# Kernel tuning notes

Hardware: AMD Instinct MI355X
Metric: run time of the kernel (lower is better)

The kernel has to match this reference:

```python
import jax, jax.numpy as jnp
import numpy as np
import math

EMBED_DIM = 128
NUM_HEADS = 16
HEAD_DIM = EMBED_DIM // NUM_HEADS  # = 8 = n_wires of the quantum circuit


def setup_inputs() -> dict:
    key = jax.random.key(0)
    k1, k2, k3 = jax.random.split(key, 3)
    B, S = 4, 2048
    x = jax.random.normal(k1, (B, S, EMBED_DIM), dtype=jnp.float32)
    # shared trainable RX angles of the single q_layer (applied to every head)
    theta = jax.random.normal(k2, (HEAD_DIM,), dtype=jnp.float32)
    w_out = jax.random.normal(k3, (EMBED_DIM, EMBED_DIM), dtype=jnp.float32) / math.sqrt(EMBED_DIM)
    mask = jnp.ones((B, S), dtype=jnp.int32)
    return {"x": x, "theta": theta, "w_out": w_out, "mask": mask}


def quantum_linear(x_head, theta):
    # Circuit: RX(x_i) encode + RX(theta_i) on wire i, CNOT chain (i, i+1),
    # then <Z_j>. For product state |psi_i> = RX(phi_i)|0>, <Z_i> = cos(phi_i),
    # and the CNOT chain gives final <Z_j> = prod_{i<=j} cos(phi_i).
    phi = x_head + theta  # [..., D] broadcast over leading dims
    return jnp.cumprod(jnp.cos(phi), axis=-1)


def reference(x, theta, w_out, mask):
    B, S, E = x.shape
    H, D = NUM_HEADS, HEAD_DIM
    xs = x.reshape(B, S, H, D)
    q = quantum_linear(xs, theta).transpose(0, 2, 1, 3)  # [B, H, S, D]; k = v = q
    scores = jnp.einsum("bhsd,bhtd->bhst", q, q) / math.sqrt(D)
    scores = jnp.where(mask[:, None, None, :] == 0, -1e9, scores)
    probs = jax.nn.softmax(scores, axis=-1)  # dropout is identity in eval
    attn = jnp.einsum("bhst,bhtd->bhsd", probs, q)
    attn = attn.transpose(0, 2, 1, 3).reshape(B, S, E)
    return attn @ w_out.T
```

## Files before the change

kernel.cpp:

```cpp
#include <hip/hip_runtime.h>
#include <hip/hip_bf16.h>
#include <hip/hip_fp16.h>

#define NB 4
#define NS 2048
#define NE 128
#define NH 16
#define ND 8

typedef __attribute__((ext_vector_type(8))) _Float16 half8;
typedef __attribute__((ext_vector_type(4))) float f32x4;

#define VSTRIDE 2056

__device__ __forceinline__ unsigned int pkrtz(float a, float b) {
    typedef __fp16 fp16v2 __attribute__((ext_vector_type(2)));
    union { fp16v2 h; unsigned int u; } v;
    v.h = __builtin_amdgcn_cvt_pkrtz(a, b);
    return v.u;
}
__device__ __forceinline__ unsigned short f2h(float a) {
    return __half_as_ushort(__float2half(a));
}
__device__ __forceinline__ half8 mk_half8(unsigned u0, unsigned u1,
                                          unsigned u2, unsigned u3) {
    union { half8 h; unsigned u[4]; } v;
    v.u[0] = u0; v.u[1] = u1; v.u[2] = u2; v.u[3] = u3;
    return v.h;
}

__global__ __launch_bounds__(512) void attn_kernel(
        const float* __restrict__ x,
        const float* __restrict__ theta,
        const int* __restrict__ mask,
        unsigned short* __restrict__ mid) {
    __shared__ unsigned short qhl[NS * ND + 24];
    __shared__ unsigned short vT[9 * VSTRIDE];
    __shared__ float kb[NS];

    const int bid = blockIdx.x;
    const int bh = bid >> 3;
    const int b = bh >> 4, h = bh & (NH - 1);
    const int meighth = bid & 7;
    const int tid = threadIdx.x;

    const float SC = 0.71421629f;

    float th[ND];
#pragma unroll
    for (int d = 0; d < ND; d++) th[d] = theta[d];

    for (int idx = tid; idx < 1024; idx += 512) {
        int chs = idx >> 4, i = idx & 15;
        int ta = 4 * (i >> 2) + 2 * (i & 1) + 16 * ((i >> 1) & 1);
        int r0 = chs * 32 + ta, r1 = r0 + 1;
        float p0[ND], p1[ND];
        {
            const float* xp = x + ((size_t)(b * NS + r0) * NE + h * ND);
            float4 a = *(const float4*)xp, c = *(const float4*)(xp + 4);
            float p = 1.f;
            p *= cosf(a.x + th[0]); p0[0] = p; p *= cosf(a.y + th[1]); p0[1] = p;
            p *= cosf(a.z + th[2]); p0[2] = p; p *= cosf(a.w + th[3]); p0[3] = p;
            p *= cosf(c.x + th[4]); p0[4] = p; p *= cosf(c.y + th[5]); p0[5] = p;
            p *= cosf(c.z + th[6]); p0[6] = p; p *= cosf(c.w + th[7]); p0[7] = p;
        }
        {
            const float* xp = x + ((size_t)(b * NS + r1) * NE + h * ND);
            float4 a = *(const float4*)xp, c = *(const float4*)(xp + 4);
            float p = 1.f;
            p *= cosf(a.x + th[0]); p1[0] = p; p *= cosf(a.y + th[1]); p1[1] = p;
            p *= cosf(a.z + th[2]); p1[2] = p; p *= cosf(a.w + th[3]); p1[3] = p;
            p *= cosf(c.x + th[4]); p1[4] = p; p *= cosf(c.y + th[5]); p1[5] = p;
            p *= cosf(c.z + th[6]); p1[6] = p; p *= cosf(c.w + th[7]); p1[7] = p;
        }
        uint4 qa, qb;
        qa.x = pkrtz(p0[0] * SC, p0[1] * SC);
        qa.y = pkrtz(p0[2] * SC, p0[3] * SC);
        qa.z = pkrtz(p0[4] * SC, p0[5] * SC);
        qa.w = pkrtz(p0[6] * SC, p0[7] * SC);
        qb.x = pkrtz(p1[0] * SC, p1[1] * SC);
        qb.y = pkrtz(p1[2] * SC, p1[3] * SC);
        qb.z = pkrtz(p1[4] * SC, p1[5] * SC);
        qb.w = pkrtz(p1[6] * SC, p1[7] * SC);
        *(uint4*)&qhl[r0 * ND] = qa;
        *(uint4*)&qhl[r1 * ND] = qb;
#pragma unroll
        for (int d = 0; d < ND; d++)
            *(unsigned int*)&vT[d * VSTRIDE + chs * 32 + 2 * i] = pkrtz(p0[d], p1[d]);
        *(unsigned int*)&vT[8 * VSTRIDE + chs * 32 + 2 * i] = 0x3C003C00u;
    }
    for (int i = tid; i < NS; i += 512)
        kb[i] = mask[b * NS + i] ? 0.f : -30000.f;
    if (tid < 24) qhl[NS * ND + tid] = 0;
    __syncthreads();

    const int wave = tid >> 6, lane = tid & 63;
    const int quad = lane >> 4, l15 = lane & 15;
    const int mbase = meighth * 256 + wave * 32;

    half8 hz = {0, 0, 0, 0, 0, 0, 0, 0};
    half8 bm0 = quad ? hz : *(const half8*)&qhl[(mbase + l15) * ND];
    half8 bm1 = quad ? hz : *(const half8*)&qhl[(mbase + 16 + l15) * ND];

    const int vrow = (l15 < 9) ? l15 : 8;
    const unsigned short* vbase = &vT[vrow * VSTRIDE];

    f32x4 O0 = {0.f, 0.f, 0.f, 0.f}, O1 = {0.f, 0.f, 0.f, 0.f};
    for (int ch = 0; ch < 64; ch++) {
        int tb = ch * 32;
        half8 at0 = *(const half8*)&qhl[(tb + l15) * ND + quad * 8];
        half8 at1 = *(const half8*)&qhl[(tb + 16 + l15) * ND + quad * 8];
        half8 vf  = *(const half8*)&vbase[tb + quad * 8];
        f32x4 C0 = *(const f32x4*)&kb[tb + quad * 4];
        f32x4 C1 = *(const f32x4*)&kb[tb + 16 + quad * 4];

        f32x4 s00 = __builtin_amdgcn_mfma_f32_16x16x32_f16(at0, bm0, C0, 0, 0, 0);
        f32x4 s01 = __builtin_amdgcn_mfma_f32_16x16x32_f16(at0, bm1, C0, 0, 0, 0);
        f32x4 s10 = __builtin_amdgcn_mfma_f32_16x16x32_f16(at1, bm0, C1, 0, 0, 0);
        f32x4 s11 = __builtin_amdgcn_mfma_f32_16x16x32_f16(at1, bm1, C1, 0, 0, 0);

        half8 pA0 = mk_half8(
            pkrtz(__builtin_amdgcn_exp2f(s00[0]), __builtin_amdgcn_exp2f(s00[1])),
            pkrtz(__builtin_amdgcn_exp2f(s00[2]), __builtin_amdgcn_exp2f(s00[3])),
            pkrtz(__builtin_amdgcn_exp2f(s10[0]), __builtin_amdgcn_exp2f(s10[1])),
            pkrtz(__builtin_amdgcn_exp2f(s10[2]), __builtin_amdgcn_exp2f(s10[3])));
        half8 pA1 = mk_half8(
            pkrtz(__builtin_amdgcn_exp2f(s01[0]), __builtin_amdgcn_exp2f(s01[1])),
            pkrtz(__builtin_amdgcn_exp2f(s01[2]), __builtin_amdgcn_exp2f(s01[3])),
            pkrtz(__builtin_amdgcn_exp2f(s11[0]), __builtin_amdgcn_exp2f(s11[1])),
            pkrtz(__builtin_amdgcn_exp2f(s11[2]), __builtin_amdgcn_exp2f(s11[3])));

        O0 = __builtin_amdgcn_mfma_f32_16x16x32_f16(pA0, vf, O0, 0, 0, 0);
        O1 = __builtin_amdgcn_mfma_f32_16x16x32_f16(pA1, vf, O1, 0, 0, 0);
    }

#pragma unroll
    for (int mt = 0; mt < 2; mt++) {
        f32x4 O = mt ? O1 : O0;
#pragma unroll
        for (int r = 0; r < 4; r++) {
            float lsum = __shfl(O[r], (lane & 48) | 8, 64);
            float v = O[r] / lsum;
            if (l15 < ND) {
                int m = mbase + mt * 16 + quad * 4 + r;
                mid[(size_t)(b * NS + m) * NE + h * ND + l15] = f2h(v);
            }
        }
    }
}

__global__ __launch_bounds__(256) void proj_kernel(
        const unsigned short* __restrict__ mid,
        const float* __restrict__ w,
        float* __restrict__ out) {
    __shared__ unsigned short wf[NE * 136];
    __shared__ unsigned short am[32 * 136];
    const int rb = blockIdx.x * 32;
    const int tid = threadIdx.x;

    for (int i = tid; i < 2048; i += 256) {
        const float* wp = w + i * 8;
        float4 a = *(const float4*)wp, c = *(const float4*)(wp + 4);
        uint4 pk;
        pk.x = pkrtz(a.x, a.y); pk.y = pkrtz(a.z, a.w);
        pk.z = pkrtz(c.x, c.y); pk.w = pkrtz(c.z, c.w);
        int n = i >> 4, k8 = (i & 15) * 8;
        *(uint4*)&wf[n * 136 + k8] = pk;
    }
    for (int i = tid; i < 512; i += 256) {
        int r = i >> 4, k8 = (i & 15) * 8;
        uint4 v = *(const uint4*)&mid[(size_t)(rb + r) * NE + k8];
        *(uint4*)&am[r * 136 + k8] = v;
    }
    __syncthreads();

    const int wave = tid >> 6, lane = tid & 63;
    const int quad = lane >> 4, l15 = lane & 15;
    const int mt = wave & 1, nh = wave >> 1;

    half8 af[4];
#pragma unroll
    for (int kt = 0; kt < 4; kt++)
        af[kt] = *(const half8*)&am[(mt * 16 + l15) * 136 + kt * 32 + quad * 8];

#pragma unroll
    for (int nt = 0; nt < 4; nt++) {
        int n0 = (nh * 4 + nt) * 16;
        f32x4 acc = {0.f, 0.f, 0.f, 0.f};
#pragma unroll
        for (int kt = 0; kt < 4; kt++) {
            half8 bf = *(const half8*)&wf[(n0 + l15) * 136 + kt * 32 + quad * 8];
            acc = __builtin_amdgcn_mfma_f32_16x16x32_f16(af[kt], bf, acc, 0, 0, 0);
        }
#pragma unroll
        for (int r = 0; r < 4; r++)
            out[(size_t)(rb + mt * 16 + quad * 4 + r) * NE + n0 + l15] = acc[r];
    }
}

extern "C" void kernel_launch(void* const* d_in, const int* in_sizes, int n_in,
                              void* d_out, int out_size, void* d_ws, size_t ws_size,
                              hipStream_t stream) {
    const float* x     = (const float*)d_in[0];
    const float* theta = (const float*)d_in[1];
    const float* w_out = (const float*)d_in[2];
    const int*   mask  = (const int*)d_in[3];
    float* out = (float*)d_out;

    unsigned short* mid16 = (unsigned short*)d_ws;

    attn_kernel<<<NB * NH * 8, 512, 0, stream>>>(x, theta, mask, mid16);
    proj_kernel<<<NB * NS / 32, 256, 0, stream>>>(mid16, w_out, out);
}
```

Baseline: 102.7 us.

## Split key/value staging into two halves and fold mask into values

The attention kernel now stages keys and values in two 1024-row halves instead of the full 2048-row sequence, which shrinks shared memory so more blocks can be resident, with a launch bound of 8. The mask is applied by zeroing masked rows' value and row-sum entries rather than adding a bias array to the score MFMA accumulator, which removes the kb shared buffer and its per-chunk loads. Query rows for the block are computed once into a small separate buffer. The cost is an extra barrier between halves. Masked keys now contribute zero instead of exp(-large), so a row whose keys are all masked would divide by zero.

```diff
diff --git a/kernel.cpp b/kernel.cpp
--- a/kernel.cpp
+++ b/kernel.cpp
@@ -11,7 +11,7 @@
 typedef __attribute__((ext_vector_type(8))) _Float16 half8;
 typedef __attribute__((ext_vector_type(4))) float f32x4;
 
-#define VSTRIDE 2056
+#define VSTRIDEH 1032
 
 __device__ __forceinline__ unsigned int pkrtz(float a, float b) {
     typedef __fp16 fp16v2 __attribute__((ext_vector_type(2)));
@@ -28,15 +28,23 @@
     v.u[0] = u0; v.u[1] = u1; v.u[2] = u2; v.u[3] = u3;
     return v.h;
 }
-
-__global__ __launch_bounds__(512) void attn_kernel(
+__device__ __forceinline__ void qrow(const float* xp, const float* th, float* p) {
+    float4 a = *(const float4*)xp, c = *(const float4*)(xp + 4);
+    float t = 1.f;
+    t *= cosf(a.x + th[0]); p[0] = t; t *= cosf(a.y + th[1]); p[1] = t;
+    t *= cosf(a.z + th[2]); p[2] = t; t *= cosf(a.w + th[3]); p[3] = t;
+    t *= cosf(c.x + th[4]); p[4] = t; t *= cosf(c.y + th[5]); p[5] = t;
+    t *= cosf(c.z + th[6]); p[6] = t; t *= cosf(c.w + th[7]); p[7] = t;
+}
+
+__global__ __launch_bounds__(512, 8) void attn_kernel(
         const float* __restrict__ x,
         const float* __restrict__ theta,
         const int* __restrict__ mask,
         unsigned short* __restrict__ mid) {
-    __shared__ unsigned short qhl[NS * ND + 24];
-    __shared__ unsigned short vT[9 * VSTRIDE];
-    __shared__ float kb[NS];
+    __shared__ unsigned short qt[1024 * ND + 24];
+    __shared__ unsigned short vTh[9 * VSTRIDEH];
+    __shared__ unsigned short qm[256 * ND + 8];
 
     const int bid = blockIdx.x;
     const int bh = bid >> 3;
@@ -50,90 +58,91 @@
 #pragma unroll
     for (int d = 0; d < ND; d++) th[d] = theta[d];
 
-    for (int idx = tid; idx < 1024; idx += 512) {
-        int chs = idx >> 4, i = idx & 15;
-        int ta = 4 * (i >> 2) + 2 * (i & 1) + 16 * ((i >> 1) & 1);
-        int r0 = chs * 32 + ta, r1 = r0 + 1;
-        float p0[ND], p1[ND];
-        {
-            const float* xp = x + ((size_t)(b * NS + r0) * NE + h * ND);
-            float4 a = *(const float4*)xp, c = *(const float4*)(xp + 4);
-            float p = 1.f;
-            p *= cosf(a.x + th[0]); p0[0] = p; p *= cosf(a.y + th[1]); p0[1] = p;
-            p *= cosf(a.z + th[2]); p0[2] = p; p *= cosf(a.w + th[3]); p0[3] = p;
-            p *= cosf(c.x + th[4]); p0[4] = p; p *= cosf(c.y + th[5]); p0[5] = p;
-            p *= cosf(c.z + th[6]); p0[6] = p; p *= cosf(c.w + th[7]); p0[7] = p;
-        }
-        {
-            const float* xp = x + ((size_t)(b * NS + r1) * NE + h * ND);
-            float4 a = *(const float4*)xp, c = *(const float4*)(xp + 4);
-            float p = 1.f;
-            p *= cosf(a.x + th[0]); p1[0] = p; p *= cosf(a.y + th[1]); p1[1] = p;
-            p *= cosf(a.z + th[2]); p1[2] = p; p *= cosf(a.w + th[3]); p1[3] = p;
-            p *= cosf(c.x + th[4]); p1[4] = p; p *= cosf(c.y + th[5]); p1[5] = p;
-            p *= cosf(c.z + th[6]); p1[6] = p; p *= cosf(c.w + th[7]); p1[7] = p;
-        }
-        uint4 qa, qb;
-        qa.x = pkrtz(p0[0] * SC, p0[1] * SC);
-        qa.y = pkrtz(p0[2] * SC, p0[3] * SC);
-        qa.z = pkrtz(p0[4] * SC, p0[5] * SC);
-        qa.w = pkrtz(p0[6] * SC, p0[7] * SC);
-        qb.x = pkrtz(p1[0] * SC, p1[1] * SC);
-        qb.y = pkrtz(p1[2] * SC, p1[3] * SC);
-        qb.z = pkrtz(p1[4] * SC, p1[5] * SC);
-        qb.w = pkrtz(p1[6] * SC, p1[7] * SC);
-        *(uint4*)&qhl[r0 * ND] = qa;
-        *(uint4*)&qhl[r1 * ND] = qb;
-#pragma unroll
-        for (int d = 0; d < ND; d++)
-            *(unsigned int*)&vT[d * VSTRIDE + chs * 32 + 2 * i] = pkrtz(p0[d], p1[d]);
-        *(unsigned int*)&vT[8 * VSTRIDE + chs * 32 + 2 * i] = 0x3C003C00u;
-    }
-    for (int i = tid; i < NS; i += 512)
-        kb[i] = mask[b * NS + i] ? 0.f : -30000.f;
-    if (tid < 24) qhl[NS * ND + tid] = 0;
-    __syncthreads();
+    if (tid < 256) {
+        int m = meighth * 256 + tid;
+        float pm[ND];
+        qrow(x + ((size_t)(b * NS + m) * NE + h * ND), th, pm);
+        uint4 qa;
+        qa.x = pkrtz(pm[0] * SC, pm[1] * SC);
+        qa.y = pkrtz(pm[2] * SC, pm[3] * SC);
+        qa.z = pkrtz(pm[4] * SC, pm[5] * SC);
+        qa.w = pkrtz(pm[6] * SC, pm[7] * SC);
+        *(uint4*)&qm[tid * ND] = qa;
+    }
+    if (tid < 24) qt[1024 * ND + tid] = 0;
 
     const int wave = tid >> 6, lane = tid & 63;
     const int quad = lane >> 4, l15 = lane & 15;
+    const int vrow = (l15 < 9) ? l15 : 8;
+    const unsigned short* vbase = &vTh[vrow * VSTRIDEH];
+    half8 hz = {0, 0, 0, 0, 0, 0, 0, 0};
+
+    const int chs = tid >> 4, si = tid & 15;
+    const int ta = 4 * (si >> 2) + 2 * (si & 1) + 16 * ((si >> 1) & 1);
+    const int r0l = chs * 32 + ta;
+
+    f32x4 O0 = {0.f, 0.f, 0.f, 0.f}, O1 = {0.f, 0.f, 0.f, 0.f};
+
+    for (int p = 0; p < 2; p++) {
+        if (p) __syncthreads();
+        {
+            int t0 = p * 1024 + r0l, t1 = t0 + 1;
+            float p0[ND], p1[ND];
+            qrow(x + ((size_t)(b * NS + t0) * NE + h * ND), th, p0);
+            qrow(x + ((size_t)(b * NS + t1) * NE + h * ND), th, p1);
+            float sk0 = mask[b * NS + t0] ? SC : 0.f;
+            float sk1 = mask[b * NS + t1] ? SC : 0.f;
+            uint4 qa, qb;
+            qa.x = pkrtz(p0[0] * SC, p0[1] * SC);
+            qa.y = pkrtz(p0[2] * SC, p0[3] * SC);
+            qa.z = pkrtz(p0[4] * SC, p0[5] * SC);
+            qa.w = pkrtz(p0[6] * SC, p0[7] * SC);
+            qb.x = pkrtz(p1[0] * SC, p1[1] * SC);
+            qb.y = pkrtz(p1[2] * SC, p1[3] * SC);
+            qb.z = pkrtz(p1[4] * SC, p1[5] * SC);
+            qb.w = pkrtz(p1[6] * SC, p1[7] * SC);
+            *(uint4*)&qt[r0l * ND]       = qa;
+            *(uint4*)&qt[(r0l + 1) * ND] = qb;
+#pragma unroll
+            for (int d = 0; d < ND; d++)
+                *(unsigned int*)&vTh[d * VSTRIDEH + chs * 32 + 2 * si] =
+                    pkrtz(p0[d] * sk0, p1[d] * sk1);
+            *(unsigned int*)&vTh[8 * VSTRIDEH + chs * 32 + 2 * si] = pkrtz(sk0, sk1);
+        }
+        __syncthreads();
+
+        half8 bm0 = quad ? hz : *(const half8*)&qm[(wave * 32 + l15) * ND];
+        half8 bm1 = quad ? hz : *(const half8*)&qm[(wave * 32 + 16 + l15) * ND];
+
+        for (int ch = 0; ch < 32; ch++) {
+            int tbl = ch * 32;
+            half8 at0 = *(const half8*)&qt[(tbl + l15) * ND + quad * 8];
+            half8 at1 = *(const half8*)&qt[(tbl + 16 + l15) * ND + quad * 8];
+            half8 vf  = *(const half8*)&vbase[tbl + quad * 8];
+            f32x4 z = {0.f, 0.f, 0.f, 0.f};
+
+            f32x4 s00 = __builtin_amdgcn_mfma_f32_16x16x32_f16(at0, bm0, z, 0, 0, 0);
+            f32x4 s01 = __builtin_amdgcn_mfma_f32_16x16x32_f16(at0, bm1, z, 0, 0, 0);
+            f32x4 s10 = __builtin_amdgcn_mfma_f32_16x16x32_f16(at1, bm0, z, 0, 0, 0);
+            f32x4 s11 = __builtin_amdgcn_mfma_f32_16x16x32_f16(at1, bm1, z, 0, 0, 0);
+
+            half8 pA0 = mk_half8(
+                pkrtz(__builtin_amdgcn_exp2f(s00[0]), __builtin_amdgcn_exp2f(s00[1])),
+                pkrtz(__builtin_amdgcn_exp2f(s00[2]), __builtin_amdgcn_exp2f(s00[3])),
+                pkrtz(__builtin_amdgcn_exp2f(s10[0]), __builtin_amdgcn_exp2f(s10[1])),
+                pkrtz(__builtin_amdgcn_exp2f(s10[2]), __builtin_amdgcn_exp2f(s10[3])));
+            half8 pA1 = mk_half8(
+                pkrtz(__builtin_amdgcn_exp2f(s01[0]), __builtin_amdgcn_exp2f(s01[1])),
+                pkrtz(__builtin_amdgcn_exp2f(s01[2]), __builtin_amdgcn_exp2f(s01[3])),
+                pkrtz(__builtin_amdgcn_exp2f(s11[0]), __builtin_amdgcn_exp2f(s11[1])),
+                pkrtz(__builtin_amdgcn_exp2f(s11[2]), __builtin_amdgcn_exp2f(s11[3])));
+
+            O0 = __builtin_amdgcn_mfma_f32_16x16x32_f16(pA0, vf, O0, 0, 0, 0);
+            O1 = __builtin_amdgcn_mfma_f32_16x16x32_f16(pA1, vf, O1, 0, 0, 0);
+        }
+    }
+
     const int mbase = meighth * 256 + wave * 32;
-
-    half8 hz = {0, 0, 0, 0, 0, 0, 0, 0};
-    half8 bm0 = quad ? hz : *(const half8*)&qhl[(mbase + l15) * ND];
-    half8 bm1 = quad ? hz : *(const half8*)&qhl[(mbase + 16 + l15) * ND];
-
-    const int vrow = (l15 < 9) ? l15 : 8;
-    const unsigned short* vbase = &vT[vrow * VSTRIDE];
-
-    f32x4 O0 = {0.f, 0.f, 0.f, 0.f}, O1 = {0.f, 0.f, 0.f, 0.f};
-    for (int ch = 0; ch < 64; ch++) {
-        int tb = ch * 32;
-        half8 at0 = *(const half8*)&qhl[(tb + l15) * ND + quad * 8];
-        half8 at1 = *(const half8*)&qhl[(tb + 16 + l15) * ND + quad * 8];
-        half8 vf  = *(const half8*)&vbase[tb + quad * 8];
-        f32x4 C0 = *(const f32x4*)&kb[tb + quad * 4];
-        f32x4 C1 = *(const f32x4*)&kb[tb + 16 + quad * 4];
-
-        f32x4 s00 = __builtin_amdgcn_mfma_f32_16x16x32_f16(at0, bm0, C0, 0, 0, 0);
-        f32x4 s01 = __builtin_amdgcn_mfma_f32_16x16x32_f16(at0, bm1, C0, 0, 0, 0);
-        f32x4 s10 = __builtin_amdgcn_mfma_f32_16x16x32_f16(at1, bm0, C1, 0, 0, 0);
-        f32x4 s11 = __builtin_amdgcn_mfma_f32_16x16x32_f16(at1, bm1, C1, 0, 0, 0);
-
-        half8 pA0 = mk_half8(
-            pkrtz(__builtin_amdgcn_exp2f(s00[0]), __builtin_amdgcn_exp2f(s00[1])),
-            pkrtz(__builtin_amdgcn_exp2f(s00[2]), __builtin_amdgcn_exp2f(s00[3])),
-            pkrtz(__builtin_amdgcn_exp2f(s10[0]), __builtin_amdgcn_exp2f(s10[1])),
-            pkrtz(__builtin_amdgcn_exp2f(s10[2]), __builtin_amdgcn_exp2f(s10[3])));
-        half8 pA1 = mk_half8(
-            pkrtz(__builtin_amdgcn_exp2f(s01[0]), __builtin_amdgcn_exp2f(s01[1])),
-            pkrtz(__builtin_amdgcn_exp2f(s01[2]), __builtin_amdgcn_exp2f(s01[3])),
-            pkrtz(__builtin_amdgcn_exp2f(s11[0]), __builtin_amdgcn_exp2f(s11[1])),
-            pkrtz(__builtin_amdgcn_exp2f(s11[2]), __builtin_amdgcn_exp2f(s11[3])));
-
-        O0 = __builtin_amdgcn_mfma_f32_16x16x32_f16(pA0, vf, O0, 0, 0, 0);
-        O1 = __builtin_amdgcn_mfma_f32_16x16x32_f16(pA1, vf, O1, 0, 0, 0);
-    }
-
 #pragma unroll
     for (int mt = 0; mt < 2; mt++) {
         f32x4 O = mt ? O1 : O0;
```

Measured after the change: 110.7 us. 1.08x slower.
